# Kernel tuning notes

Measured on AMD Instinct MI355X. Metric: run time of the kernel, lower is better.

## Reference

```python
import jax, jax.numpy as jnp
import numpy as np

N_NODES = 100000
N_EDGES = 1200000
HID = 64
EDGE_DIM = 16
N_LAYERS = 3


def setup_inputs() -> dict:
    key = jax.random.key(0)
    ks = jax.random.split(key, 16)
    s = 0.1  # weight scale
    return {
        'node_features': jax.random.normal(ks[0], (N_NODES, HID), jnp.float32),
        'edge_index': jax.random.randint(ks[1], (2, N_EDGES), 0, N_NODES, jnp.int32),
        'edge_features': jax.random.normal(ks[2], (N_EDGES, EDGE_DIM), jnp.float32),
        'enc_W': jax.random.normal(ks[3], (HID, HID), jnp.float32) * s,
        'enc_b': jnp.zeros((HID,), jnp.float32),
        'msg_W1': jax.random.normal(ks[4], (N_LAYERS, 2 * HID + EDGE_DIM, HID), jnp.float32) * s,
        'msg_b1': jnp.zeros((N_LAYERS, HID), jnp.float32),
        'msg_W2': jax.random.normal(ks[5], (N_LAYERS, HID, HID), jnp.float32) * s,
        'msg_b2': jnp.zeros((N_LAYERS, HID), jnp.float32),
        'gru_Wih': jax.random.normal(ks[6], (N_LAYERS, HID, 3 * HID), jnp.float32) * s,
        'gru_Whh': jax.random.normal(ks[7], (N_LAYERS, HID, 3 * HID), jnp.float32) * s,
        'gru_bih': jnp.zeros((N_LAYERS, 3 * HID), jnp.float32),
        'gru_bhh': jnp.zeros((N_LAYERS, 3 * HID), jnp.float32),
        'ro_W1': jax.random.normal(ks[8], (HID, HID), jnp.float32) * s,
        'ro_b1': jnp.zeros((HID,), jnp.float32),
        'ro_W2': jax.random.normal(ks[9], (HID, HID), jnp.float32) * s,
        'ro_b2': jnp.zeros((HID,), jnp.float32),
    }


def _gru_cell(x, h, Wih, Whh, bih, bhh):
    # torch GRUCell, gate order (r, z, n)
    gi = x @ Wih + bih  # [N, 3H]
    gh = h @ Whh + bhh
    gi_r, gi_z, gi_n = jnp.split(gi, 3, axis=-1)
    gh_r, gh_z, gh_n = jnp.split(gh, 3, axis=-1)
    r = jax.nn.sigmoid(gi_r + gh_r)
    z = jax.nn.sigmoid(gi_z + gh_z)
    n = jnp.tanh(gi_n + r * gh_n)
    return (1.0 - z) * n + z * h


def reference(node_features, edge_index, edge_features, enc_W, enc_b,
              msg_W1, msg_b1, msg_W2, msg_b2,
              gru_Wih, gru_Whh, gru_bih, gru_bhh,
              ro_W1, ro_b1, ro_W2, ro_b2):
    src, dst = edge_index[0], edge_index[1]
    n_nodes = node_features.shape[0]
    h = node_features @ enc_W + enc_b  # node encoder (no relu in graph path)
    for l in range(N_LAYERS):
        cat = jnp.concatenate([h[src], h[dst], edge_features], axis=-1)  # [E, 2H+Ed]
        m = jax.nn.relu(cat @ msg_W1[l] + msg_b1[l]) @ msg_W2[l] + msg_b2[l]  # [E, H]
        agg = jax.ops.segment_sum(m, dst, num_segments=n_nodes)  # scatter-add
        h = _gru_cell(agg, h, gru_Wih[l], gru_Whh[l], gru_bih[l], gru_bhh[l])
    return jax.nn.relu(h @ ro_W1 + ro_b1) @ ro_W2 + ro_b2
```

## Files before the change

kernel.cpp:

```cpp
#include <hip/hip_runtime.h>
#include <hip/hip_bf16.h>
#include <math.h>

#define HIDDIM 64
#define EDIM 16

typedef _Float16 h16;
typedef __attribute__((ext_vector_type(8))) _Float16 half8v;
typedef __attribute__((ext_vector_type(4))) float f32x4;
typedef unsigned int uint32;

template<int K, int N, int EPI, int RELU>
__global__ __launch_bounds__(256) void mfma_gemm_kernel(
    const float* __restrict__ A0, const float* __restrict__ A1,
    const h16* __restrict__ Bp, const float* __restrict__ bias,
    float* __restrict__ outf, h16* __restrict__ outP,
    h16* __restrict__ outQ, float* __restrict__ hbuf,
    const int* __restrict__ row_start, const float* __restrict__ b2ih, int M)
{
    constexpr int KP = K + 8;
    constexpr int NT = N / 16;
    constexpr int KC = K / 32;
    constexpr int R8 = K / 8;
    __shared__ __align__(16) h16 Asub[64 * KP];

    const int mbase = blockIdx.x * 64;
    const int tid = threadIdx.x;
    const int wid = tid >> 6, lane = tid & 63;

    constexpr int ITERS = 64 * R8 / 256;
#pragma unroll
    for (int it = 0; it < ITERS; ++it) {
        int e8 = tid + it * 256;
        int row = e8 / R8;
        int col = (e8 - row * R8) * 8;
        int grow = mbase + row;
        float v[8];
        if (grow < M) {
            const float* sp;
            if (EPI == 2) {
                sp = (col < 64) ? (A0 + (size_t)grow * 64 + col)
                                : (A1 + (size_t)grow * 64 + (col - 64));
            } else {
                sp = A0 + (size_t)grow * K + col;
            }
            f32x4 a = *(const f32x4*)sp;
            f32x4 b = *(const f32x4*)(sp + 4);
            v[0] = a.x; v[1] = a.y; v[2] = a.z; v[3] = a.w;
            v[4] = b.x; v[5] = b.y; v[6] = b.z; v[7] = b.w;
        } else {
#pragma unroll
            for (int i = 0; i < 8; ++i) v[i] = 0.f;
        }
        half8v hv;
#pragma unroll
        for (int i = 0; i < 8; ++i) hv[i] = (h16)v[i];
        *(half8v*)&Asub[row * KP + col] = hv;
    }
    __syncthreads();

    const int colb = lane & 15;
    f32x4 acc[NT];
#pragma unroll
    for (int t = 0; t < NT; ++t) {
        float bv = bias ? bias[t * 16 + colb] : 0.f;
        acc[t].x = bv; acc[t].y = bv; acc[t].z = bv; acc[t].w = bv;
    }
    const int aoff = (wid * 16 + colb) * KP + (lane >> 4) * 8;
    const half8v* Bv = (const half8v*)Bp;
#pragma unroll
    for (int c = 0; c < KC; ++c) {
        half8v af = *(const half8v*)&Asub[aoff + c * 32];
#pragma unroll
        for (int t = 0; t < NT; ++t) {
            half8v bf = Bv[(t * KC + c) * 64 + lane];
            acc[t] = __builtin_amdgcn_mfma_f32_16x16x32_f16(af, bf, acc[t], 0, 0, 0);
        }
    }

    if (EPI == 0) {
#pragma unroll
        for (int r = 0; r < 4; ++r) {
            int row = mbase + wid * 16 + (lane >> 4) * 4 + r;
            if (row < M) {
#pragma unroll
                for (int t = 0; t < NT; ++t) {
                    float vv = acc[t][r];
                    if (RELU) vv = vv > 0.f ? vv : 0.f;
                    outf[(size_t)row * N + t * 16 + colb] = vv;
                }
            }
        }
    } else if (EPI == 1) {
#pragma unroll
        for (int r = 0; r < 4; ++r) {
            int row = mbase + wid * 16 + (lane >> 4) * 4 + r;
            if (row < M) {
#pragma unroll
                for (int t = 0; t < NT; ++t) {
                    h16 us = (h16)acc[t][r];
                    int col = t * 16 + colb;
                    if (t < 4) outP[(size_t)row * 64 + col] = us;
                    else       outQ[(size_t)row * 64 + (col - 64)] = us;
                }
            }
        }
    } else {
        float b2r[4], b2z[4], b2n[4];
#pragma unroll
        for (int j4 = 0; j4 < 4; ++j4) {
            int j = j4 * 16 + colb;
            b2r[j4] = b2ih[j];
            b2z[j4] = b2ih[64 + j];
            b2n[j4] = b2ih[128 + j];
        }
#pragma unroll
        for (int r = 0; r < 4; ++r) {
            int row = mbase + wid * 16 + (lane >> 4) * 4 + r;
            if (row < M) {
                float deg = (float)(row_start[row + 1] - row_start[row]);
#pragma unroll
                for (int j4 = 0; j4 < 4; ++j4) {
                    float rv = acc[j4][r] + deg * b2r[j4];
                    rv = 1.f / (1.f + __expf(-rv));
                    float zv = acc[4 + j4][r] + deg * b2z[j4];
                    zv = 1.f / (1.f + __expf(-zv));
                    float gin = acc[8 + j4][r] + deg * b2n[j4];
                    float ghn = acc[12 + j4][r];
                    float nv = tanhf(gin + rv * ghn);
                    size_t off = (size_t)row * 64 + j4 * 16 + colb;
                    float hold = hbuf[off];
                    hbuf[off] = (1.f - zv) * nv + zv * hold;
                }
            }
        }
    }
}

__global__ __launch_bounds__(256) void pack_plain_kernel(
    const float* __restrict__ B, h16* __restrict__ Bp, int Kd, int Nd)
{
    int idx = blockIdx.x * 256 + threadIdx.x;
    int KC = Kd >> 5;
    int total = (Nd >> 4) * KC * 64;
    if (idx >= total) return;
    int lane = idx & 63, fc = idx >> 6;
    int t = fc / KC, c = fc - t * KC;
    int col = t * 16 + (lane & 15);
    int k0 = c * 32 + (lane >> 4) * 8;
    half8v us;
#pragma unroll
    for (int i = 0; i < 8; ++i) us[i] = (h16)B[(size_t)(k0 + i) * Nd + col];
    *(half8v*)(Bp + (size_t)idx * 8) = us;
}

__global__ __launch_bounds__(256) void pack_pq_kernel(
    const float* __restrict__ W1, h16* __restrict__ Bp)
{
    int idx = blockIdx.x * 256 + threadIdx.x;
    if (idx >= 1024) return;
    int lane = idx & 63, fc = idx >> 6;
    int t = fc >> 1, c = fc & 1;
    int n = t * 16 + (lane & 15);
    int k0 = c * 32 + (lane >> 4) * 8;
    half8v us;
#pragma unroll
    for (int i = 0; i < 8; ++i) {
        int k = k0 + i;
        float v = (n < 64) ? W1[(size_t)k * 64 + n]
                           : W1[(size_t)(64 + k) * 64 + (n - 64)];
        us[i] = (h16)v;
    }
    *(half8v*)(Bp + (size_t)idx * 8) = us;
}

__global__ __launch_bounds__(256) void pack_gru_kernel(
    const float* __restrict__ Wci, const float* __restrict__ Whh,
    h16* __restrict__ Bp)
{
    int idx = blockIdx.x * 256 + threadIdx.x;
    if (idx >= 4096) return;
    int lane = idx & 63, fc = idx >> 6;
    int t = fc >> 2, c = fc & 3;
    int n = t * 16 + (lane & 15);
    int k0 = c * 32 + (lane >> 4) * 8;
    half8v us;
#pragma unroll
    for (int i = 0; i < 8; ++i) {
        int k = k0 + i;
        float v;
        if (n < 128)      v = (k < 64) ? Wci[(size_t)k * 192 + n]
                                       : Whh[(size_t)(k - 64) * 192 + n];
        else if (n < 192) v = (k < 64) ? Wci[(size_t)k * 192 + n] : 0.f;
        else              v = (k >= 64) ? Whh[(size_t)(k - 64) * 192 + (n - 64)] : 0.f;
        us[i] = (h16)v;
    }
    *(half8v*)(Bp + (size_t)idx * 8) = us;
}

__global__ void bias_pq_kernel(const float* __restrict__ b1, float* __restrict__ out)
{
    int i = threadIdx.x;
    out[i] = (i < 64) ? 0.f : b1[i - 64];
}

__global__ void bias_gru_kernel(const float* __restrict__ bih,
                                const float* __restrict__ bhh,
                                float* __restrict__ out)
{
    int i = threadIdx.x;
    float v;
    if (i < 128)      v = bih[i] + bhh[i];
    else if (i < 192) v = bih[i];
    else              v = bhh[i - 64];
    out[i] = v;
}

__global__ __launch_bounds__(256) void count_kernel(
    const int* __restrict__ dst, int* __restrict__ cnt, int nE)
{
    int e = blockIdx.x * 256 + threadIdx.x;
    if (e >= nE) return;
    atomicAdd(&cnt[dst[e]], 1);
}

__global__ __launch_bounds__(256) void partial_kernel(
    const int* __restrict__ cnt, int* __restrict__ partial, int nNodes)
{
    __shared__ int lds[256];
    int i = blockIdx.x * 256 + threadIdx.x;
    int v = (i < nNodes) ? cnt[i] : 0;
    lds[threadIdx.x] = v;
    __syncthreads();
#pragma unroll
    for (int off = 128; off > 0; off >>= 1) {
        if (threadIdx.x < off) lds[threadIdx.x] += lds[threadIdx.x + off];
        __syncthreads();
    }
    if (threadIdx.x == 0) partial[blockIdx.x] = lds[0];
}

__global__ __launch_bounds__(1024) void scan_partials_kernel(
    int* __restrict__ partial, int* __restrict__ row_start, int nb,
    int nNodes, int nE)
{
    __shared__ int lds[1024];
    int tid = threadIdx.x;
    int v = (tid < nb) ? partial[tid] : 0;
    lds[tid] = v;
    __syncthreads();
    for (int off = 1; off < 1024; off <<= 1) {
        int t = (tid >= off) ? lds[tid - off] : 0;
        __syncthreads();
        lds[tid] += t;
        __syncthreads();
    }
    if (tid < nb) partial[tid] = lds[tid] - v;
    if (tid == 0) row_start[nNodes] = nE;
}

__global__ __launch_bounds__(256) void scan_blocks_kernel(
    const int* __restrict__ cnt, const int* __restrict__ partial,
    int* __restrict__ row_start, int* __restrict__ cursor, int nNodes)
{
    __shared__ int lds[256];
    int i = blockIdx.x * 256 + threadIdx.x;
    int v = (i < nNodes) ? cnt[i] : 0;
    lds[threadIdx.x] = v;
    __syncthreads();
    for (int off = 1; off < 256; off <<= 1) {
        int t = (threadIdx.x >= off) ? lds[threadIdx.x - off] : 0;
        __syncthreads();
        lds[threadIdx.x] += t;
        __syncthreads();
    }
    if (i < nNodes) {
        int excl = partial[blockIdx.x] + lds[threadIdx.x] - v;
        row_start[i] = excl;
        cursor[i] = excl;
    }
}

__global__ __launch_bounds__(256) void fill_kernel(
    const int* __restrict__ src, const int* __restrict__ dst,
    const float* __restrict__ ef, int* __restrict__ cursor,
    int* __restrict__ ss, h16* __restrict__ sefh, int nE)
{
    int e = blockIdx.x * 256 + threadIdx.x;
    if (e >= nE) return;
    int d = dst[e];
    int p = atomicAdd(&cursor[d], 1);
    ss[p] = src[e];
    const float4* er = reinterpret_cast<const float4*>(ef + (size_t)e * 16);
    float4 a0 = er[0], a1 = er[1], a2 = er[2], a3 = er[3];
    half8v u0, u1;
    u0[0]=(h16)a0.x; u0[1]=(h16)a0.y; u0[2]=(h16)a0.z; u0[3]=(h16)a0.w;
    u0[4]=(h16)a1.x; u0[5]=(h16)a1.y; u0[6]=(h16)a1.z; u0[7]=(h16)a1.w;
    u1[0]=(h16)a2.x; u1[1]=(h16)a2.y; u1[2]=(h16)a2.z; u1[3]=(h16)a2.w;
    u1[4]=(h16)a3.x; u1[5]=(h16)a3.y; u1[6]=(h16)a3.z; u1[7]=(h16)a3.w;
    half8v* sr = reinterpret_cast<half8v*>(sefh + (size_t)p * 16);
    sr[0] = u0; sr[1] = u1;
}

__global__ void combine_kernel(
    const float* __restrict__ mW2, const float* __restrict__ mb2,
    const float* __restrict__ gWih, float* __restrict__ Wci,
    float* __restrict__ b2ih)
{
    int l = blockIdx.x;
    int g = threadIdx.x;
    const float* W2  = mW2  + (size_t)l * 64 * 64;
    const float* Wih = gWih + (size_t)l * 64 * 192;
    const float* b2  = mb2  + (size_t)l * 64;
    float acc[64];
#pragma unroll
    for (int k = 0; k < 64; ++k) acc[k] = 0.f;
    float bacc = 0.f;
#pragma unroll 1
    for (int j = 0; j < 64; ++j) {
        float w = Wih[j * 192 + g];
        bacc += b2[j] * w;
#pragma unroll
        for (int k = 0; k < 64; ++k) acc[k] += W2[k * 64 + j] * w;
    }
    float* o = Wci + (size_t)l * 64 * 192;
#pragma unroll
    for (int k = 0; k < 64; ++k) o[k * 192 + g] = acc[k];
    b2ih[l * 192 + g] = bacc;
}

__device__ __forceinline__ float edot(const half8v& A, const half8v& B,
                                      const float w[16])
{
    float r = 0.f;
#pragma unroll
    for (int k = 0; k < 8; ++k) r += (float)A[k] * w[k];
#pragma unroll
    for (int k = 0; k < 8; ++k) r += (float)B[k] * w[8 + k];
    return r;
}

__global__ __launch_bounds__(256) void edge_agg_kernel(
    const h16* __restrict__ Pb, const h16* __restrict__ Qb,
    float* __restrict__ T, const h16* __restrict__ sefh,
    const float* __restrict__ W1c, const int* __restrict__ sorted_src,
    const int* __restrict__ row_start, int nNodes)
{
    int wg = blockIdx.x * 4 + (threadIdx.x >> 6);
    wg = __builtin_amdgcn_readfirstlane(wg);
    int lane = threadIdx.x & 63;
    int nw = gridDim.x * 4;

    float w1c[16];
#pragma unroll
    for (int k = 0; k < 16; ++k) w1c[k] = W1c[k * 64 + lane];

    for (int n = wg; n < nNodes; n += nw) {
        int rs = row_start[n];
        int re = row_start[n + 1];
        float q = (float)Qb[(size_t)n * 64 + lane];
        float tacc = 0.f;
        int i = rs;
        for (; i + 4 <= re; i += 4) {
            int s0 = sorted_src[i + 0];
            int s1 = sorted_src[i + 1];
            int s2 = sorted_src[i + 2];
            int s3 = sorted_src[i + 3];
            float p0 = (float)Pb[(size_t)s0 * 64 + lane];
            float p1 = (float)Pb[(size_t)s1 * 64 + lane];
            float p2 = (float)Pb[(size_t)s2 * 64 + lane];
            float p3 = (float)Pb[(size_t)s3 * 64 + lane];
            const half8v* e8 = reinterpret_cast<const half8v*>(sefh + (size_t)i * 16);
            half8v c0 = e8[0], c1 = e8[1], c2 = e8[2], c3 = e8[3];
            half8v c4 = e8[4], c5 = e8[5], c6 = e8[6], c7 = e8[7];
            float r0 = edot(c0, c1, w1c);
            float r1 = edot(c2, c3, w1c);
            float r2 = edot(c4, c5, w1c);
            float r3 = edot(c6, c7, w1c);
            float t0 = p0 + q + r0; t0 = t0 > 0.f ? t0 : 0.f;
            float t1 = p1 + q + r1; t1 = t1 > 0.f ? t1 : 0.f;
            float t2 = p2 + q + r2; t2 = t2 > 0.f ? t2 : 0.f;
            float t3 = p3 + q + r3; t3 = t3 > 0.f ? t3 : 0.f;
            tacc += (t0 + t1) + (t2 + t3);
        }
        for (; i < re; ++i) {
            int s = sorted_src[i];
            float p = (float)Pb[(size_t)s * 64 + lane];
            const half8v* e8 = reinterpret_cast<const half8v*>(sefh + (size_t)i * 16);
            half8v c0 = e8[0], c1 = e8[1];
            float r = edot(c0, c1, w1c);
            float t = p + q + r;
            t = t > 0.f ? t : 0.f;
            tacc += t;
        }
        T[(size_t)n * 64 + lane] = tacc;
    }
}

extern "C" void kernel_launch(void* const* d_in, const int* in_sizes, int n_in,
                              void* d_out, int out_size, void* d_ws, size_t ws_size,
                              hipStream_t stream)
{
    const float* nf    = (const float*)d_in[0];
    const int*   ei    = (const int*)  d_in[1];
    const float* ef    = (const float*)d_in[2];
    const float* enc_W = (const float*)d_in[3];
    const float* enc_b = (const float*)d_in[4];
    const float* mW1   = (const float*)d_in[5];
    const float* mb1   = (const float*)d_in[6];
    const float* mW2   = (const float*)d_in[7];
    const float* mb2   = (const float*)d_in[8];
    const float* gWih  = (const float*)d_in[9];
    const float* gWhh  = (const float*)d_in[10];
    const float* gbih  = (const float*)d_in[11];
    const float* gbhh  = (const float*)d_in[12];
    const float* rW1   = (const float*)d_in[13];
    const float* rb1   = (const float*)d_in[14];
    const float* rW2   = (const float*)d_in[15];
    const float* rb2   = (const float*)d_in[16];

    const int N = in_sizes[0] / HIDDIM;
    const int E = in_sizes[2] / EDIM;

    char* wsB = (char*)d_ws;
    auto alloc = [&](size_t bytes) {
        char* p = wsB;
        wsB += (bytes + 255) & ~(size_t)255;
        return p;
    };
    float* h          = (float*)alloc((size_t)N * 64 * 4);
    float* T          = (float*)alloc((size_t)N * 64 * 4);
    float* Rt         = (float*)alloc((size_t)N * 64 * 4);
    h16*  Pb          = (h16*)alloc((size_t)N * 64 * 2);
    h16*  Qb          = (h16*)alloc((size_t)N * 64 * 2);
    int*   row_start  = (int*)alloc((size_t)(N + 1) * 4);
    int*   cursor     = (int*)alloc((size_t)N * 4);
    int*   cnt        = (int*)alloc((size_t)N * 4);
    int*   partial    = (int*)alloc(1024 * 4);
    int*   s_src      = (int*)alloc((size_t)E * 4);
    h16*  sefh        = (h16*)alloc((size_t)E * 16 * 2);
    float* Wci        = (float*)alloc(3 * 64 * 192 * 4);
    float* b2ih       = (float*)alloc(3 * 192 * 4);
    h16*  encP        = (h16*)alloc(512 * 8 * 2);
    h16*  pqP         = (h16*)alloc(3 * 1024 * 8 * 2);
    h16*  gruP        = (h16*)alloc(3 * 4096 * 8 * 2);
    h16*  ro1P        = (h16*)alloc(512 * 8 * 2);
    h16*  ro2P        = (h16*)alloc(512 * 8 * 2);
    float* bias128    = (float*)alloc(3 * 128 * 4);
    float* bias256    = (float*)alloc(3 * 256 * 4);

    const int gemmGrid = (N + 63) / 64;
    const int edgeGrid = (E + 255) / 256;
    const int nScanBlk = (N + 255) / 256;

    hipMemsetAsync(cnt, 0, (size_t)N * 4, stream);
    count_kernel<<<edgeGrid, 256, 0, stream>>>(ei + E, cnt, E);
    partial_kernel<<<nScanBlk, 256, 0, stream>>>(cnt, partial, N);
    scan_partials_kernel<<<1, 1024, 0, stream>>>(partial, row_start, nScanBlk, N, E);
    scan_blocks_kernel<<<nScanBlk, 256, 0, stream>>>(cnt, partial, row_start, cursor, N);
    fill_kernel<<<edgeGrid, 256, 0, stream>>>(ei, ei + E, ef, cursor, s_src, sefh, E);

    combine_kernel<<<3, 192, 0, stream>>>(mW2, mb2, gWih, Wci, b2ih);
    pack_plain_kernel<<<2, 256, 0, stream>>>(enc_W, encP, 64, 64);
    pack_plain_kernel<<<2, 256, 0, stream>>>(rW1, ro1P, 64, 64);
    pack_plain_kernel<<<2, 256, 0, stream>>>(rW2, ro2P, 64, 64);
    for (int l = 0; l < 3; ++l) {
        pack_pq_kernel<<<4, 256, 0, stream>>>(mW1 + (size_t)l * 144 * 64,
                                              pqP + (size_t)l * 1024 * 8);
        pack_gru_kernel<<<16, 256, 0, stream>>>(Wci + (size_t)l * 64 * 192,
                                                gWhh + (size_t)l * 64 * 192,
                                                gruP + (size_t)l * 4096 * 8);
        bias_pq_kernel<<<1, 128, 0, stream>>>(mb1 + (size_t)l * 64,
                                              bias128 + (size_t)l * 128);
        bias_gru_kernel<<<1, 256, 0, stream>>>(gbih + (size_t)l * 192,
                                               gbhh + (size_t)l * 192,
                                               bias256 + (size_t)l * 256);
    }

    mfma_gemm_kernel<64, 64, 0, 0><<<gemmGrid, 256, 0, stream>>>(
        nf, nullptr, encP, enc_b, h, nullptr, nullptr, nullptr, nullptr, nullptr, N);

    for (int l = 0; l < 3; ++l) {
        mfma_gemm_kernel<64, 128, 1, 0><<<gemmGrid, 256, 0, stream>>>(
            h, nullptr, pqP + (size_t)l * 1024 * 8, bias128 + (size_t)l * 128,
            nullptr, Pb, Qb, nullptr, nullptr, nullptr, N);
        edge_agg_kernel<<<2048, 256, 0, stream>>>(
            Pb, Qb, T, sefh, mW1 + (size_t)l * 144 * 64 + 128 * 64,
            s_src, row_start, N);
        mfma_gemm_kernel<128, 256, 2, 0><<<gemmGrid, 256, 0, stream>>>(
            T, h, gruP + (size_t)l * 4096 * 8, bias256 + (size_t)l * 256,
            nullptr, nullptr, nullptr, h, row_start, b2ih + (size_t)l * 192, N);
    }

    mfma_gemm_kernel<64, 64, 0, 1><<<gemmGrid, 256, 0, stream>>>(
        h, nullptr, ro1P, rb1, Rt, nullptr, nullptr, nullptr, nullptr, nullptr, N);
    mfma_gemm_kernel<64, 64, 0, 0><<<gemmGrid, 256, 0, stream>>>(
        Rt, nullptr, ro2P, rb2, (float*)d_out, nullptr, nullptr, nullptr,
        nullptr, nullptr, N);
}
```

Measured before the change: 882.4 us.

## Store node state and intermediates in fp16 and use fdot2 in edge aggregation

Converts the hidden state h, the aggregated buffer T and the readout intermediate from fp32 to fp16 storage. This halves global traffic in the GEMM and edge kernels, and the GEMM loaders now read half8 directly instead of converting floats. The edge kernel packs the edge-feature weights as fp16 pairs, uses the fdot2 builtin for the 16-wide edge dot product, and adds an 8-edge unrolled loop. The cost is lower precision: h is rounded to fp16 every layer, so error builds up across layers.

```diff
diff --git a/kernel.cpp b/kernel.cpp
--- a/kernel.cpp
+++ b/kernel.cpp
@@ -7,54 +7,63 @@
 
 typedef _Float16 h16;
 typedef __attribute__((ext_vector_type(8))) _Float16 half8v;
+typedef __attribute__((ext_vector_type(2))) _Float16 half2v;
 typedef __attribute__((ext_vector_type(4))) float f32x4;
 typedef unsigned int uint32;
 
-template<int K, int N, int EPI, int RELU>
+#if defined(__has_builtin)
+#if __has_builtin(__builtin_amdgcn_fdot2)
+#define HAS_FDOT2 1
+#endif
+#endif
+
+template<int K, int N, int EPI, int RELU, int AF32>
 __global__ __launch_bounds__(256) void mfma_gemm_kernel(
-    const float* __restrict__ A0, const float* __restrict__ A1,
-    const h16* __restrict__ Bp, const float* __restrict__ bias,
-    float* __restrict__ outf, h16* __restrict__ outP,
-    h16* __restrict__ outQ, float* __restrict__ hbuf,
+    const float* __restrict__ A0f, const h16* __restrict__ A0h,
+    const h16* __restrict__ A1h, const h16* __restrict__ Bp,
+    const float* __restrict__ bias, float* __restrict__ outf,
+    h16* __restrict__ outh, h16* __restrict__ outQ, h16* __restrict__ hbuf,
     const int* __restrict__ row_start, const float* __restrict__ b2ih, int M)
 {
     constexpr int KP = K + 8;
     constexpr int NT = N / 16;
     constexpr int KC = K / 32;
-    constexpr int R8 = K / 8;
     __shared__ __align__(16) h16 Asub[64 * KP];
 
     const int mbase = blockIdx.x * 64;
     const int tid = threadIdx.x;
     const int wid = tid >> 6, lane = tid & 63;
 
-    constexpr int ITERS = 64 * R8 / 256;
+    constexpr int C8 = K / 8;
+    constexpr int ITERS = 64 * C8 / 256;
 #pragma unroll
     for (int it = 0; it < ITERS; ++it) {
-        int e8 = tid + it * 256;
-        int row = e8 / R8;
-        int col = (e8 - row * R8) * 8;
+        int idx = tid + it * 256;
+        int row = idx / C8;
+        int col = (idx - row * C8) * 8;
         int grow = mbase + row;
-        float v[8];
+        half8v hv;
         if (grow < M) {
-            const float* sp;
-            if (EPI == 2) {
-                sp = (col < 64) ? (A0 + (size_t)grow * 64 + col)
-                                : (A1 + (size_t)grow * 64 + (col - 64));
+            if (AF32) {
+                const float* sp = A0f + (size_t)grow * K + col;
+                f32x4 a = *(const f32x4*)sp;
+                f32x4 b = *(const f32x4*)(sp + 4);
+                hv[0]=(h16)a.x; hv[1]=(h16)a.y; hv[2]=(h16)a.z; hv[3]=(h16)a.w;
+                hv[4]=(h16)b.x; hv[5]=(h16)b.y; hv[6]=(h16)b.z; hv[7]=(h16)b.w;
             } else {
-                sp = A0 + (size_t)grow * K + col;
-            }
-            f32x4 a = *(const f32x4*)sp;
-            f32x4 b = *(const f32x4*)(sp + 4);
-            v[0] = a.x; v[1] = a.y; v[2] = a.z; v[3] = a.w;
-            v[4] = b.x; v[5] = b.y; v[6] = b.z; v[7] = b.w;
+                const h16* sp;
+                if (EPI == 3) {
+                    sp = (col < 64) ? (A0h + (size_t)grow * 64 + col)
+                                    : (A1h + (size_t)grow * 64 + (col - 64));
+                } else {
+                    sp = A0h + (size_t)grow * K + col;
+                }
+                hv = *(const half8v*)sp;
+            }
         } else {
 #pragma unroll
-            for (int i = 0; i < 8; ++i) v[i] = 0.f;
-        }
-        half8v hv;
-#pragma unroll
-        for (int i = 0; i < 8; ++i) hv[i] = (h16)v[i];
+            for (int i = 0; i < 8; ++i) hv[i] = (h16)0.f;
+        }
         *(half8v*)&Asub[row * KP + col] = hv;
     }
     __syncthreads();
@@ -98,9 +107,22 @@
             if (row < M) {
 #pragma unroll
                 for (int t = 0; t < NT; ++t) {
+                    float vv = acc[t][r];
+                    if (RELU) vv = vv > 0.f ? vv : 0.f;
+                    outh[(size_t)row * N + t * 16 + colb] = (h16)vv;
+                }
+            }
+        }
+    } else if (EPI == 2) {
+#pragma unroll
+        for (int r = 0; r < 4; ++r) {
+            int row = mbase + wid * 16 + (lane >> 4) * 4 + r;
+            if (row < M) {
+#pragma unroll
+                for (int t = 0; t < NT; ++t) {
                     h16 us = (h16)acc[t][r];
                     int col = t * 16 + colb;
-                    if (t < 4) outP[(size_t)row * 64 + col] = us;
+                    if (t < 4) outh[(size_t)row * 64 + col] = us;
                     else       outQ[(size_t)row * 64 + (col - 64)] = us;
                 }
             }
@@ -129,8 +151,8 @@
                     float ghn = acc[12 + j4][r];
                     float nv = tanhf(gin + rv * ghn);
                     size_t off = (size_t)row * 64 + j4 * 16 + colb;
-                    float hold = hbuf[off];
-                    hbuf[off] = (1.f - zv) * nv + zv * hold;
+                    float hold = (float)hbuf[off];
+                    hbuf[off] = (h16)((1.f - zv) * nv + zv * hold);
                 }
             }
         }
@@ -196,6 +218,15 @@
         us[i] = (h16)v;
     }
     *(half8v*)(Bp + (size_t)idx * 8) = us;
+}
+
+__global__ __launch_bounds__(256) void pack_w1c_kernel(
+    const float* __restrict__ mW1, h16* __restrict__ w1ch)
+{
+    int idx = blockIdx.x * 256 + threadIdx.x;
+    if (idx >= 3 * 1024) return;
+    int l = idx >> 10, r = idx & 1023;
+    w1ch[idx] = (h16)mW1[(size_t)l * 144 * 64 + 128 * 64 + r];
 }
 
 __global__ void bias_pq_kernel(const float* __restrict__ b1, float* __restrict__ out)
@@ -329,21 +360,30 @@
     b2ih[l * 192 + g] = bacc;
 }
 
-__device__ __forceinline__ float edot(const half8v& A, const half8v& B,
-                                      const float w[16])
-{
-    float r = 0.f;
-#pragma unroll
-    for (int k = 0; k < 8; ++k) r += (float)A[k] * w[k];
-#pragma unroll
-    for (int k = 0; k < 8; ++k) r += (float)B[k] * w[8 + k];
+__device__ __forceinline__ float edot16(half8v a, half8v b, const half2v w[8],
+                                        float seed)
+{
+    float r = seed;
+#if defined(HAS_FDOT2)
+    const half2v* ap = (const half2v*)&a;
+    const half2v* bp = (const half2v*)&b;
+#pragma unroll
+    for (int j = 0; j < 4; ++j) r = __builtin_amdgcn_fdot2(ap[j], w[j], r, false);
+#pragma unroll
+    for (int j = 0; j < 4; ++j) r = __builtin_amdgcn_fdot2(bp[j], w[4 + j], r, false);
+#else
+#pragma unroll
+    for (int k = 0; k < 8; ++k) r += (float)a[k] * (float)w[k >> 1][k & 1];
+#pragma unroll
+    for (int k = 0; k < 8; ++k) r += (float)b[k] * (float)w[4 + (k >> 1)][k & 1];
+#endif
     return r;
 }
 
 __global__ __launch_bounds__(256) void edge_agg_kernel(
     const h16* __restrict__ Pb, const h16* __restrict__ Qb,
-    float* __restrict__ T, const h16* __restrict__ sefh,
-    const float* __restrict__ W1c, const int* __restrict__ sorted_src,
+    h16* __restrict__ T, const h16* __restrict__ sefh,
+    const h16* __restrict__ w1ch, const int* __restrict__ sorted_src,
     const int* __restrict__ row_start, int nNodes)
 {
     int wg = blockIdx.x * 4 + (threadIdx.x >> 6);
@@ -351,9 +391,14 @@
     int lane = threadIdx.x & 63;
     int nw = gridDim.x * 4;
 
-    float w1c[16];
-#pragma unroll
-    for (int k = 0; k < 16; ++k) w1c[k] = W1c[k * 64 + lane];
+    half2v w2[8];
+#pragma unroll
+    for (int j = 0; j < 8; ++j) {
+        half2v p;
+        p[0] = w1ch[(2 * j) * 64 + lane];
+        p[1] = w1ch[(2 * j + 1) * 64 + lane];
+        w2[j] = p;
+    }
 
     for (int n = wg; n < nNodes; n += nw) {
         int rs = row_start[n];
@@ -361,39 +406,45 @@
         float q = (float)Qb[(size_t)n * 64 + lane];
         float tacc = 0.f;
         int i = rs;
+        for (; i + 8 <= re; i += 8) {
+            float p[8];
+#pragma unroll
+            for (int j = 0; j < 8; ++j) {
+                int s = sorted_src[i + j];
+                p[j] = (float)Pb[(size_t)s * 64 + lane];
+            }
+            const half8v* e8 = reinterpret_cast<const half8v*>(sefh + (size_t)i * 16);
+#pragma unroll
+            for (int j = 0; j < 8; ++j) {
+                float t = edot16(e8[2 * j], e8[2 * j + 1], w2, p[j] + q);
+                t = t > 0.f ? t : 0.f;
+                tacc += t;
+            }
+        }
         for (; i + 4 <= re; i += 4) {
-            int s0 = sorted_src[i + 0];
-            int s1 = sorted_src[i + 1];
-            int s2 = sorted_src[i + 2];
-            int s3 = sorted_src[i + 3];
-            float p0 = (float)Pb[(size_t)s0 * 64 + lane];
-            float p1 = (float)Pb[(size_t)s1 * 64 + lane];
-            float p2 = (float)Pb[(size_t)s2 * 64 + lane];
-            float p3 = (float)Pb[(size_t)s3 * 64 + lane];
+            float p[4];
+#pragma unroll
+            for (int j = 0; j < 4; ++j) {
+                int s = sorted_src[i + j];
+                p[j] = (float)Pb[(size_t)s * 64 + lane];
+            }
             const half8v* e8 = reinterpret_cast<const half8v*>(sefh + (size_t)i * 16);
-            half8v c0 = e8[0], c1 = e8[1], c2 = e8[2], c3 = e8[3];
-            half8v c4 = e8[4], c5 = e8[5], c6 = e8[6], c7 = e8[7];
-            float r0 = edot(c0, c1, w1c);
-            float r1 = edot(c2, c3, w1c);
-            float r2 = edot(c4, c5, w1c);
-            float r3 = edot(c6, c7, w1c);
-            float t0 = p0 + q + r0; t0 = t0 > 0.f ? t0 : 0.f;
-            float t1 = p1 + q + r1; t1 = t1 > 0.f ? t1 : 0.f;
-            float t2 = p2 + q + r2; t2 = t2 > 0.f ? t2 : 0.f;
-            float t3 = p3 + q + r3; t3 = t3 > 0.f ? t3 : 0.f;
-            tacc += (t0 + t1) + (t2 + t3);
+#pragma unroll
+            for (int j = 0; j < 4; ++j) {
+                float t = edot16(e8[2 * j], e8[2 * j + 1], w2, p[j] + q);
+                t = t > 0.f ? t : 0.f;
+                tacc += t;
+            }
         }
         for (; i < re; ++i) {
             int s = sorted_src[i];
             float p = (float)Pb[(size_t)s * 64 + lane];
             const half8v* e8 = reinterpret_cast<const half8v*>(sefh + (size_t)i * 16);
-            half8v c0 = e8[0], c1 = e8[1];
-            float r = edot(c0, c1, w1c);
-            float t = p + q + r;
+            float t = edot16(e8[0], e8[1], w2, p + q);
             t = t > 0.f ? t : 0.f;
             tacc += t;
         }
-        T[(size_t)n * 64 + lane] = tacc;
+        T[(size_t)n * 64 + lane] = (h16)tacc;
     }
 }
 
@@ -428,9 +479,9 @@
         wsB += (bytes + 255) & ~(size_t)255;
         return p;
     };
-    float* h          = (float*)alloc((size_t)N * 64 * 4);
-    float* T          = (float*)alloc((size_t)N * 64 * 4);
-    float* Rt         = (float*)alloc((size_t)N * 64 * 4);
+    h16*  h           = (h16*)alloc((size_t)N * 64 * 2);
+    h16*  T           = (h16*)alloc((size_t)N * 64 * 2);
+    h16*  Rt          = (h16*)alloc((size_t)N * 64 * 2);
     h16*  Pb          = (h16*)alloc((size_t)N * 64 * 2);
     h16*  Qb          = (h16*)alloc((size_t)N * 64 * 2);
     int*   row_start  = (int*)alloc((size_t)(N + 1) * 4);
@@ -446,6 +497,7 @@
     h16*  gruP        = (h16*)alloc(3 * 4096 * 8 * 2);
     h16*  ro1P        = (h16*)alloc(512 * 8 * 2);
     h16*  ro2P        = (h16*)alloc(512 * 8 * 2);
+    h16*  w1ch        = (h16*)alloc(3 * 1024 * 2);
     float* bias128    = (float*)alloc(3 * 128 * 4);
     float* bias256    = (float*)alloc(3 * 256 * 4);
 
@@ -464,6 +516,7 @@
     pack_plain_kernel<<<2, 256, 0, stream>>>(enc_W, encP, 64, 64);
     pack_plain_kernel<<<2, 256, 0, stream>>>(rW1, ro1P, 64, 64);
     pack_plain_kernel<<<2, 256, 0, stream>>>(rW2, ro2P, 64, 64);
+    pack_w1c_kernel<<<12, 256, 0, stream>>>(mW1, w1ch);
     for (int l = 0; l < 3; ++l) {
         pack_pq_kernel<<<4, 256, 0, stream>>>(mW1 + (size_t)l * 144 * 64,
                                               pqP + (size_t)l * 1024 * 8);
@@ -477,24 +530,27 @@
                                                bias256 + (size_t)l * 256);
     }
 
-    mfma_gemm_kernel<64, 64, 0, 0><<<gemmGrid, 256, 0, stream>>>(
-        nf, nullptr, encP, enc_b, h, nullptr, nullptr, nullptr, nullptr, nullptr, N);
+    mfma_gemm_kernel<64, 64, 1, 0, 1><<<gemmGrid, 256, 0, stream>>>(
+        nf, nullptr, nullptr, encP, enc_b, nullptr, h, nullptr, nullptr,
+        nullptr, nullptr, N);
 
     for (int l = 0; l < 3; ++l) {
-        mfma_gemm_kernel<64, 128, 1, 0><<<gemmGrid, 256, 0, stream>>>(
-            h, nullptr, pqP + (size_t)l * 1024 * 8, bias128 + (size_t)l * 128,
-            nullptr, Pb, Qb, nullptr, nullptr, nullptr, N);
+        mfma_gemm_kernel<64, 128, 2, 0, 0><<<gemmGrid, 256, 0, stream>>>(
+            nullptr, h, nullptr, pqP + (size_t)l * 1024 * 8,
+            bias128 + (size_t)l * 128, nullptr, Pb, Qb, nullptr,
+            nullptr, nullptr, N);
         edge_agg_kernel<<<2048, 256, 0, stream>>>(
-            Pb, Qb, T, sefh, mW1 + (size_t)l * 144 * 64 + 128 * 64,
-            s_src, row_start, N);
-        mfma_gemm_kernel<128, 256, 2, 0><<<gemmGrid, 256, 0, stream>>>(
-            T, h, gruP + (size_t)l * 4096 * 8, bias256 + (size_t)l * 256,
-            nullptr, nullptr, nullptr, h, row_start, b2ih + (size_t)l * 192, N);
-    }
-
-    mfma_gemm_kernel<64, 64, 0, 1><<<gemmGrid, 256, 0, stream>>>(
-        h, nullptr, ro1P, rb1, Rt, nullptr, nullptr, nullptr, nullptr, nullptr, N);
-    mfma_gemm_kernel<64, 64, 0, 0><<<gemmGrid, 256, 0, stream>>>(
-        Rt, nullptr, ro2P, rb2, (float*)d_out, nullptr, nullptr, nullptr,
+            Pb, Qb, T, sefh, w1ch + (size_t)l * 1024, s_src, row_start, N);
+        mfma_gemm_kernel<128, 256, 3, 0, 0><<<gemmGrid, 256, 0, stream>>>(
+            nullptr, T, h, gruP + (size_t)l * 4096 * 8,
+            bias256 + (size_t)l * 256, nullptr, nullptr, nullptr, h,
+            row_start, b2ih + (size_t)l * 192, N);
+    }
+
+    mfma_gemm_kernel<64, 64, 1, 1, 0><<<gemmGrid, 256, 0, stream>>>(
+        nullptr, h, nullptr, ro1P, rb1, nullptr, Rt, nullptr, nullptr,
         nullptr, nullptr, N);
-}
+    mfma_gemm_kernel<64, 64, 0, 0, 0><<<gemmGrid, 256, 0, stream>>>(
+        nullptr, Rt, nullptr, ro2P, rb2, (float*)d_out, nullptr, nullptr,
+        nullptr, nullptr, nullptr, N);
+}
```

After: 824.6 us. 6.5% less time.
